# Kernel optimization log

Hardware: AMD Instinct MI355X
Metric: run time of the kernel (lower is better)

## Reference

```python
import jax, jax.numpy as jnp
import numpy as np


def setup_inputs() -> dict:
    key = jax.random.key(0)
    # B=32 single-channel 2048x2048 images (see shape_source)
    x = jax.random.normal(key, (32, 1, 2048, 2048), dtype=jnp.float32)
    return {"x": x}


def reference(x):
    # 2x2 pixel-unshuffle (space-to-depth). The torch module applies four
    # stride-2 conv2d calls with one-hot 2x2 kernels selecting positions
    # (0,0), (0,1), (1,0), (1,1) of each 2x2 block, concatenating on the
    # channel dim. Equivalent to a strided gather:
    return jnp.concatenate(
        [
            x[:, :, 0::2, 0::2],  # kernel [[1,0],[0,0]]
            x[:, :, 0::2, 1::2],  # kernel [[0,1],[0,0]]
            x[:, :, 1::2, 0::2],  # kernel [[0,0],[1,0]]
            x[:, :, 1::2, 1::2],  # kernel [[0,0],[0,1]]
        ],
        axis=1,
    )  # [B, 4*C, H/2, W/2]
```

## Files before the change

kernel.cpp:

```cpp
#include <hip/hip_runtime.h>


__global__ __launch_bounds__(256) void pixel_unshuffle_kernel(
    const float4* __restrict__ in4, float4* __restrict__ out4, int n_items) {
    const int stride = gridDim.x * blockDim.x;
    for (int t = blockIdx.x * blockDim.x + threadIdx.x; t < n_items; t += stride) {
        const int wi  = t & 255;
        const int row = t >> 8;
        const int h   = row & 2047;
        const int b   = row >> 11;

        const float4 a = in4[2 * t + 0];
        const float4 c = in4[2 * t + 1];

        const float4 ev = make_float4(a.x, a.z, c.x, c.z);
        const float4 od = make_float4(a.y, a.w, c.y, c.w);

        const int i     = h >> 1;
        const int cbase = (h & 1) << 1;
        const int obase = (((b << 2) + cbase) << 18) + (i << 8) + wi;

        out4[obase]          = ev;
        out4[obase + 262144] = od;
    }
}

extern "C" void kernel_launch(void* const* d_in, const int* in_sizes, int n_in,
                              void* d_out, int out_size, void* d_ws, size_t ws_size,
                              hipStream_t stream) {
    const float4* in4 = (const float4*)d_in[0];
    float4* out4      = (float4*)d_out;

    const int n_items = 32 * 2048 * 2048 / 8;
    const int block   = 256;
    const int grid    = 2048;

    pixel_unshuffle_kernel<<<grid, block, 0, stream>>>(in4, out4, n_items);
}
```

Measured before the change: 231.3 us.

## Use nontemporal float4 loads with 4-way unroll and float2 output stores

Each thread now handles four independent float4 input chunks per iteration, each read with a nontemporal load, and writes the even and odd pairs as float2 nontemporal stores. This puts more memory requests in flight per thread and keeps streaming data from polluting the cache. The cost is that each output store is half as wide, which doubles the number of store instructions.

```diff
diff --git a/kernel.cpp b/kernel.cpp
--- a/kernel.cpp
+++ b/kernel.cpp
@@ -1,39 +1,59 @@
 #include <hip/hip_runtime.h>
 
 
+typedef float f32x4 __attribute__((ext_vector_type(4)));
+typedef float f32x2 __attribute__((ext_vector_type(2)));
+
+__device__ __forceinline__ void proc_item(
+    int f, f32x4 v, f32x2* __restrict__ out2) {
+    const int col = f & 511;
+    const int row = f >> 9;
+    const int h   = row & 2047;
+    const int b   = row >> 11;
+    const int i   = h >> 1;
+    const int c   = (h & 1) << 1;
+    const int off = (((b << 2) + c) << 19) + (i << 9) + col;
+
+    f32x2 ev, od;
+    ev.x = v.x; ev.y = v.z;
+    od.x = v.y; od.y = v.w;
+
+    __builtin_nontemporal_store(ev, out2 + off);
+    __builtin_nontemporal_store(od, out2 + off + (1 << 19));
+}
+
 __global__ __launch_bounds__(256) void pixel_unshuffle_kernel(
-    const float4* __restrict__ in4, float4* __restrict__ out4, int n_items) {
-    const int stride = gridDim.x * blockDim.x;
-    for (int t = blockIdx.x * blockDim.x + threadIdx.x; t < n_items; t += stride) {
-        const int wi  = t & 255;
-        const int row = t >> 8;
-        const int h   = row & 2047;
-        const int b   = row >> 11;
+    const f32x4* __restrict__ in4, f32x2* __restrict__ out2, int n4) {
+    const int tpb  = 256;
+    const int span = gridDim.x * tpb * 4;
+    for (int base = blockIdx.x * tpb * 4 + threadIdx.x; base < n4;
+         base += span) {
+        const int f0 = base;
+        const int f1 = base + tpb;
+        const int f2 = base + 2 * tpb;
+        const int f3 = base + 3 * tpb;
 
-        const float4 a = in4[2 * t + 0];
-        const float4 c = in4[2 * t + 1];
+        const f32x4 v0 = __builtin_nontemporal_load(in4 + f0);
+        const f32x4 v1 = __builtin_nontemporal_load(in4 + f1);
+        const f32x4 v2 = __builtin_nontemporal_load(in4 + f2);
+        const f32x4 v3 = __builtin_nontemporal_load(in4 + f3);
 
-        const float4 ev = make_float4(a.x, a.z, c.x, c.z);
-        const float4 od = make_float4(a.y, a.w, c.y, c.w);
-
-        const int i     = h >> 1;
-        const int cbase = (h & 1) << 1;
-        const int obase = (((b << 2) + cbase) << 18) + (i << 8) + wi;
-
-        out4[obase]          = ev;
-        out4[obase + 262144] = od;
+        proc_item(f0, v0, out2);
+        proc_item(f1, v1, out2);
+        proc_item(f2, v2, out2);
+        proc_item(f3, v3, out2);
     }
 }
 
 extern "C" void kernel_launch(void* const* d_in, const int* in_sizes, int n_in,
                               void* d_out, int out_size, void* d_ws, size_t ws_size,
                               hipStream_t stream) {
-    const float4* in4 = (const float4*)d_in[0];
-    float4* out4      = (float4*)d_out;
+    const f32x4* in4 = (const f32x4*)d_in[0];
+    f32x2* out2      = (f32x2*)d_out;
 
-    const int n_items = 32 * 2048 * 2048 / 8;
-    const int block   = 256;
-    const int grid    = 2048;
+    const int n4    = 32 * 2048 * 2048 / 4;
+    const int block = 256;
+    const int grid  = 2048;
 
-    pixel_unshuffle_kernel<<<grid, block, 0, stream>>>(in4, out4, n_items);
+    pixel_unshuffle_kernel<<<grid, block, 0, stream>>>(in4, out2, n4);
 }
```

New measurement: 208.3 us. -10.0%, faster.

## Transpose pixel-unshuffle through LDS with coalesced nontemporal loads and prefetch

Applied to the files above, without the earlier changes.

Each wavefront now loads contiguous 1 KB chunks with fully coalesced nontemporal float4 loads and scatters the even and odd pixels into a per-wave LDS region. It then reads back contiguous float4 runs and writes them with nontemporal stores. The next chunk's loads are issued before the LDS round-trip so global latency overlaps the shuffle. The aim is to replace the old stride-2 per-thread float4 loads with unit-stride accesses and to bypass cache pollution. The cost is extra LDS traffic and a hand-placed waitcnt and scheduling barrier, which may be fragile.

```diff
diff --git a/kernel.cpp b/kernel.cpp
--- a/kernel.cpp
+++ b/kernel.cpp
@@ -1,39 +1,95 @@
 #include <hip/hip_runtime.h>
 
 
-__global__ __launch_bounds__(256) void pixel_unshuffle_kernel(
-    const float4* __restrict__ in4, float4* __restrict__ out4, int n_items) {
-    const int stride = gridDim.x * blockDim.x;
-    for (int t = blockIdx.x * blockDim.x + threadIdx.x; t < n_items; t += stride) {
-        const int wi  = t & 255;
-        const int row = t >> 8;
-        const int h   = row & 2047;
-        const int b   = row >> 11;
+typedef float f32x4 __attribute__((ext_vector_type(4)));
+typedef float f32x2 __attribute__((ext_vector_type(2)));
 
-        const float4 a = in4[2 * t + 0];
-        const float4 c = in4[2 * t + 1];
+#define NTL(p)    __builtin_nontemporal_load(p)
+#define NTS(v, p) __builtin_nontemporal_store(v, p)
 
-        const float4 ev = make_float4(a.x, a.z, c.x, c.z);
-        const float4 od = make_float4(a.y, a.w, c.y, c.w);
+__device__ __forceinline__ int ev_off(int c, int lane) {
+    const int row = c >> 2;
+    const int q   = c & 3;
+    const int h   = row & 2047;
+    const int b   = row >> 11;
+    const int i   = h >> 1;
+    const int cb  = (h & 1) << 1;
+    return (((b << 2) + cb) << 18) + (i << 8) + (q << 6) + lane;
+}
 
-        const int i     = h >> 1;
-        const int cbase = (h & 1) << 1;
-        const int obase = (((b << 2) + cbase) << 18) + (i << 8) + wi;
+__global__ __launch_bounds__(256) void pixel_unshuffle_ws(
+    const f32x4* __restrict__ in4, f32x4* __restrict__ out4, int nchunk) {
+    __shared__ alignas(16) f32x2 lds2[2048];
+    const int tid  = threadIdx.x;
+    const int wid  = tid >> 6;
+    const int lane = tid & 63;
+    f32x2* W        = lds2 + (wid << 9);
+    const f32x4* W4 = (const f32x4*)W;
 
-        out4[obase]          = ev;
-        out4[obase + 262144] = od;
+    const int gw     = (blockIdx.x << 2) + wid;
+    const int stride = gridDim.x << 3;
+
+    int c = gw << 1;
+    if (c >= nchunk) return;
+
+    f32x4 v0 = NTL(in4 + (c << 7) + lane);
+    f32x4 v1 = NTL(in4 + (c << 7) + 64 + lane);
+    f32x4 v2 = NTL(in4 + (c << 7) + 128 + lane);
+    f32x4 v3 = NTL(in4 + (c << 7) + 192 + lane);
+
+    while (true) {
+        asm volatile("" ::: "memory");
+
+        f32x2 t;
+        t.x = v0.x; t.y = v0.z; W[lane]       = t;
+        t.x = v0.y; t.y = v0.w; W[lane + 128] = t;
+        t.x = v1.x; t.y = v1.z; W[lane + 64]  = t;
+        t.x = v1.y; t.y = v1.w; W[lane + 192] = t;
+        t.x = v2.x; t.y = v2.z; W[lane + 256] = t;
+        t.x = v2.y; t.y = v2.w; W[lane + 384] = t;
+        t.x = v3.x; t.y = v3.z; W[lane + 320] = t;
+        t.x = v3.y; t.y = v3.w; W[lane + 448] = t;
+
+        const int cn   = c + stride;
+        const bool more = (cn < nchunk);
+        f32x4 u0, u1, u2, u3;
+        if (more) {
+            u0 = NTL(in4 + (cn << 7) + lane);
+            u1 = NTL(in4 + (cn << 7) + 64 + lane);
+            u2 = NTL(in4 + (cn << 7) + 128 + lane);
+            u3 = NTL(in4 + (cn << 7) + 192 + lane);
+        }
+
+        asm volatile("s_waitcnt lgkmcnt(0)" ::: "memory");
+        __builtin_amdgcn_sched_barrier(0);
+
+        const f32x4 e0 = W4[lane];
+        const f32x4 o0 = W4[lane + 64];
+        const f32x4 e1 = W4[lane + 128];
+        const f32x4 o1 = W4[lane + 192];
+
+        const int ea = ev_off(c, lane);
+        NTS(e0, out4 + ea);
+        NTS(o0, out4 + ea + (1 << 18));
+        const int eb = ev_off(c + 1, lane);
+        NTS(e1, out4 + eb);
+        NTS(o1, out4 + eb + (1 << 18));
+
+        if (!more) break;
+        v0 = u0; v1 = u1; v2 = u2; v3 = u3;
+        c = cn;
     }
 }
 
 extern "C" void kernel_launch(void* const* d_in, const int* in_sizes, int n_in,
                               void* d_out, int out_size, void* d_ws, size_t ws_size,
                               hipStream_t stream) {
-    const float4* in4 = (const float4*)d_in[0];
-    float4* out4      = (float4*)d_out;
+    const f32x4* in4 = (const f32x4*)d_in[0];
+    f32x4* out4      = (f32x4*)d_out;
 
-    const int n_items = 32 * 2048 * 2048 / 8;
-    const int block   = 256;
-    const int grid    = 2048;
+    const int nchunk = 32 * 2048 * 4;
+    const int block  = 256;
+    const int grid   = 2048;
 
-    pixel_unshuffle_kernel<<<grid, block, 0, stream>>>(in4, out4, n_items);
+    pixel_unshuffle_ws<<<grid, block, 0, stream>>>(in4, out4, nchunk);
 }
```

Measured after the change: 221.4 us. -4.3%, faster.
